# Optimization experiments

Hardware: AMD Instinct MI355X
Metric: run time of the kernel (lower is better)

Reference implementation:

```python
import jax, jax.numpy as jnp
import numpy as np

WINDOW_SIZE = 11
CHANNEL = 3
SIGMA = 1.5


def _make_window(w=WINDOW_SIZE, channel=CHANNEL, sigma=SIGMA):
    xs = np.arange(w) - w // 2
    g = np.exp(-(xs.astype(np.float64) ** 2) / (2.0 * sigma ** 2))
    g = g / g.sum()
    k2d = np.outer(g, g).astype(np.float32)  # [w,w]
    # depthwise kernel, OIHW with I=1, O=channel
    return jnp.asarray(np.broadcast_to(k2d, (channel, 1, w, w)).copy())


def setup_inputs() -> dict:
    key = jax.random.key(0)
    k1, k2 = jax.random.split(key)
    x = jax.random.uniform(k1, (32, 3, 512, 512), dtype=jnp.float32)
    y = jax.random.uniform(k2, (32, 3, 512, 512), dtype=jnp.float32)
    window = _make_window()
    return {"x": x, "y": y, "window": window}


def _dwconv(x, window):
    pad = WINDOW_SIZE // 2
    return jax.lax.conv_general_dilated(
        x, window,
        window_strides=(1, 1),
        padding=[(pad, pad), (pad, pad)],
        dimension_numbers=("NCHW", "OIHW", "NCHW"),
        feature_group_count=CHANNEL,
    )


def reference(x, y, window):
    C1 = 0.01 ** 2
    C2 = 0.03 ** 2
    mu_x = _dwconv(x, window)
    mu_y = _dwconv(y, window)
    mu_x2 = mu_x * mu_x
    mu_y2 = mu_y * mu_y
    mu_xy = mu_x * mu_y
    sigma_x2 = _dwconv(x * x, window) - mu_x2
    sigma_y2 = _dwconv(y * y, window) - mu_y2
    sigma_xy = _dwconv(x * y, window) - mu_xy
    ssim_map = ((2.0 * mu_xy + C1) * (2.0 * sigma_xy + C2)) / (
        (mu_x2 + mu_y2 + C1) * (sigma_x2 + sigma_y2 + C2)
    )
    return jnp.mean(ssim_map)
```

## Files before the change

### kernel.cpp

```cpp
#include <hip/hip_runtime.h>


#define NBLK  768
#define NSTEP 74

__device__ __forceinline__ float2 f2z() { return make_float2(0.f, 0.f); }

#define DECL_ACC(S) float2 AX##S=f2z(), AY##S=f2z(), AXX##S=f2z(), AYY##S=f2z(), AXY##S=f2z();

#define HTAP(J, EA, EB) { const float gj = g[J]; \
  { const float xv = x##EA, yv = y##EA; const float t1 = gj*xv, t2 = gj*yv; \
    sxA += t1; syA += t2; sxxA = fmaf(t1,xv,sxxA); syyA = fmaf(t2,yv,syyA); sxyA = fmaf(t1,yv,sxyA); } \
  { const float xv = x##EB, yv = y##EB; const float t1 = gj*xv, t2 = gj*yv; \
    sxB += t1; syB += t2; sxxB = fmaf(t1,xv,sxxB); syyB = fmaf(t2,yv,syyB); sxyB = fmaf(t1,yv,sxyB); } }

#define VACC(S, RR) { const float wj = g[(10 - (S) + (RR)) % 11]; \
  AX##S.x  = fmaf(wj, sxA , AX##S.x ); AX##S.y  = fmaf(wj, sxB , AX##S.y ); \
  AY##S.x  = fmaf(wj, syA , AY##S.x ); AY##S.y  = fmaf(wj, syB , AY##S.y ); \
  AXX##S.x = fmaf(wj, sxxA, AXX##S.x); AXX##S.y = fmaf(wj, sxxB, AXX##S.y); \
  AYY##S.x = fmaf(wj, syyA, AYY##S.x); AYY##S.y = fmaf(wj, syyB, AYY##S.y); \
  AXY##S.x = fmaf(wj, sxyA, AXY##S.x); AXY##S.y = fmaf(wj, sxyB, AXY##S.y); }

#define EMIT(S) { \
  { const float mux = AX##S.x, muy = AY##S.x; \
    const float mux2 = mux*mux, muy2 = muy*muy, muxy = mux*muy; \
    const float vvx = AXX##S.x - mux2, vvy = AYY##S.x - muy2, vxy = AXY##S.x - muxy; \
    const float num = fmaf(2.f, muxy, C1) * fmaf(2.f, vxy, C2); \
    const float den = (mux2 + muy2 + C1) * (vvx + vvy + C2); \
    ts.x += num * __builtin_amdgcn_rcpf(den); } \
  { const float mux = AX##S.y, muy = AY##S.y; \
    const float mux2 = mux*mux, muy2 = muy*muy, muxy = mux*muy; \
    const float vvx = AXX##S.y - mux2, vvy = AYY##S.y - muy2, vxy = AXY##S.y - muxy; \
    const float num = fmaf(2.f, muxy, C1) * fmaf(2.f, vxy, C2); \
    const float den = (mux2 + muy2 + C1) * (vvx + vvy + C2); \
    ts.y += num * __builtin_amdgcn_rcpf(den); } }

#define RESET(S) { AX##S=f2z(); AY##S=f2z(); AXX##S=f2z(); AYY##S=f2z(); AXY##S=f2z(); }

#define STEP(RR) { \
  const int i = ibase + (RR); \
  if (i < NSTEP) { \
    const int rn = r0 - 4 + i; \
    float2 mx=f2z(), my=f2z(), hx=f2z(), hy=f2z(); \
    if (i <= NSTEP-2 && (unsigned)rn < 512u) { \
      const float* xp = xplane + rn * 512; \
      const float* yp = yplane + rn * 512; \
      mx = *(const float2*)(xp + mcol); my = *(const float2*)(yp + mcol); \
      if (hOK) { hx = *(const float2*)(xp + hcol); hy = *(const float2*)(yp + hcol); } \
    } \
    const float2 xa0 = sxw[lane  ], xa1 = sxw[lane+1], xa2 = sxw[lane+2], xa3 = sxw[lane+3]; \
    const float2 xa4 = sxw[lane+4], xa5 = sxw[lane+5], xa6 = sxw[lane+6]; \
    const float2 ya0 = syw[lane  ], ya1 = syw[lane+1], ya2 = syw[lane+2], ya3 = syw[lane+3]; \
    const float2 ya4 = syw[lane+4], ya5 = syw[lane+5], ya6 = syw[lane+6]; \
    float sxA=0.f, syA=0.f, sxxA=0.f, syyA=0.f, sxyA=0.f; \
    float sxB=0.f, syB=0.f, sxxB=0.f, syyB=0.f, sxyB=0.f; \
    HTAP(0,a0.y,a1.x) HTAP(1,a1.x,a1.y) HTAP(2,a1.y,a2.x) HTAP(3,a2.x,a2.y) \
    HTAP(4,a2.y,a3.x) HTAP(5,a3.x,a3.y) HTAP(6,a3.y,a4.x) HTAP(7,a4.x,a4.y) \
    HTAP(8,a4.y,a5.x) HTAP(9,a5.x,a5.y) HTAP(10,a5.y,a6.x) \
    VACC(0,RR) VACC(1,RR) VACC(2,RR) VACC(3,RR) VACC(4,RR) VACC(5,RR) \
    VACC(6,RR) VACC(7,RR) VACC(8,RR) VACC(9,RR) VACC(10,RR) \
    if (i >= 10) { EMIT(RR) } \
    RESET(RR) \
    sxw[lane+3] = mx; syw[lane+3] = my; \
    if (isHalo) { sxw[hslot] = hx; syw[hslot] = hy; } \
  } }

__global__ __launch_bounds__(256, 2) void ssim_fused(
    const float* __restrict__ x, const float* __restrict__ y,
    const float* __restrict__ window,
    unsigned* __restrict__ counter, float* __restrict__ partials,
    float* __restrict__ out)
{
    const int tid  = threadIdx.x;
    const int lane = tid & 63;
    const int wv   = tid >> 6;
    const int W    = blockIdx.x * 4 + wv;
    const int img  = W >> 5;
    const int cb   = (W >> 3) & 3;
    const int rb   = W & 7;
    const int r0   = rb << 6;
    const int c0   = cb << 7;

    const float* xplane = x + (size_t)img * 262144;
    const float* yplane = y + (size_t)img * 262144;

    float g[11];
    #pragma unroll
    for (int ii = 0; ii < 11; ++ii) {
        float s = 0.f;
        #pragma unroll
        for (int jj = 0; jj < 11; ++jj) s += window[ii * 11 + jj];
        g[ii] = s;
    }

    __shared__ float2 lsx[4][70];
    __shared__ float2 lsy[4][70];
    float2* sxw = lsx[wv];
    float2* syw = lsy[wv];

    const bool isHalo = lane < 6;
    const int  hslot  = (lane < 3) ? lane : (64 + lane);
    const int  hcol   = (lane < 3) ? (c0 - 6 + 2 * lane)
                                   : (c0 + 128 + 2 * (lane - 3));
    const bool hOK    = isHalo && (hcol >= 0) && (hcol < 511);
    const int  mcol   = c0 + 2 * lane;

    DECL_ACC(0) DECL_ACC(1) DECL_ACC(2) DECL_ACC(3) DECL_ACC(4) DECL_ACC(5)
    DECL_ACC(6) DECL_ACC(7) DECL_ACC(8) DECL_ACC(9) DECL_ACC(10)

    {
        const int rn = r0 - 5;
        float2 mx = f2z(), my = f2z(), hx = f2z(), hy = f2z();
        if (rn >= 0) {
            const float* xp = xplane + rn * 512;
            const float* yp = yplane + rn * 512;
            mx = *(const float2*)(xp + mcol);
            my = *(const float2*)(yp + mcol);
            if (hOK) { hx = *(const float2*)(xp + hcol); hy = *(const float2*)(yp + hcol); }
        }
        sxw[lane + 3] = mx; syw[lane + 3] = my;
        if (isHalo) { sxw[hslot] = hx; syw[hslot] = hy; }
    }

    float2 ts = f2z();
    const float C1 = 1e-4f, C2 = 9e-4f;

    #pragma unroll 1
    for (int chunk = 0; chunk < 7; ++chunk) {
        const int ibase = chunk * 11;
        STEP(0) STEP(1) STEP(2) STEP(3) STEP(4) STEP(5)
        STEP(6) STEP(7) STEP(8) STEP(9) STEP(10)
    }

    float t = ts.x + ts.y;
    #pragma unroll
    for (int off = 32; off > 0; off >>= 1) t += __shfl_down(t, off, 64);
    __shared__ float wsum[4];
    __shared__ int   sflag;
    if (lane == 0) wsum[wv] = t;
    __syncthreads();
    if (tid == 0) {
        partials[blockIdx.x] = (wsum[0] + wsum[1]) + (wsum[2] + wsum[3]);
        __threadfence();
        const unsigned old = atomicAdd(counter, 1u);
        sflag = (old == NBLK - 1) ? 1 : 0;
    }
    __syncthreads();
    if (sflag) {
        __threadfence();
        double s = 0.0;
        for (int idx = tid; idx < NBLK; idx += 256) s += (double)partials[idx];
        #pragma unroll
        for (int off = 32; off > 0; off >>= 1) s += __shfl_down(s, off, 64);
        __shared__ double dsum[4];
        if (lane == 0) dsum[wv] = s;
        __syncthreads();
        if (tid == 0)
            out[0] = (float)(((dsum[0] + dsum[1]) + (dsum[2] + dsum[3])) / 25165824.0);
    }
}

extern "C" void kernel_launch(void* const* d_in, const int* in_sizes, int n_in,
                              void* d_out, int out_size, void* d_ws, size_t ws_size,
                              hipStream_t stream)
{
    const float* x = (const float*)d_in[0];
    const float* y = (const float*)d_in[1];
    const float* w = (const float*)d_in[2];
    unsigned* counter = (unsigned*)d_ws;
    float* partials   = (float*)((char*)d_ws + 256);

    hipMemsetAsync(d_ws, 0, 4, stream);
    ssim_fused<<<NBLK, 256, 0, stream>>>(x, y, w, counter, partials, (float*)d_out);
}
```

Baseline: 305.9 us.

## Use one-wave blocks with scalar Gaussian weights and wave-level final reduction

Changes the launch from 768 blocks of four waves to 3072 single-wave blocks, with each block owning one 64x128 tile. The Gaussian weights become named scalars broadcast via readfirstlane, and the vertical-tap index is resolved per step at preprocessing time, so weights can sit in SGPRs instead of a runtime-indexed array. Block-level shared-memory reductions and __syncthreads are replaced by a shuffle broadcast of the atomic counter result. Dropping the (256,2) launch bound frees the register budget, which may change occupancy. Four times as many partials must be summed in the final pass.

```diff
diff --git a/kernel.cpp b/kernel.cpp
--- a/kernel.cpp
+++ b/kernel.cpp
@@ -1,25 +1,38 @@
 #include <hip/hip_runtime.h>
 
 
-#define NBLK  768
+#define NBLK  3072
 #define NSTEP 74
 
 __device__ __forceinline__ float2 f2z() { return make_float2(0.f, 0.f); }
 
 #define DECL_ACC(S) float2 AX##S=f2z(), AY##S=f2z(), AXX##S=f2z(), AYY##S=f2z(), AXY##S=f2z();
 
-#define HTAP(J, EA, EB) { const float gj = g[J]; \
+#define HTAP(J, EA, EB) { const float gj = g##J; \
   { const float xv = x##EA, yv = y##EA; const float t1 = gj*xv, t2 = gj*yv; \
     sxA += t1; syA += t2; sxxA = fmaf(t1,xv,sxxA); syyA = fmaf(t2,yv,syyA); sxyA = fmaf(t1,yv,sxyA); } \
   { const float xv = x##EB, yv = y##EB; const float t1 = gj*xv, t2 = gj*yv; \
     sxB += t1; syB += t2; sxxB = fmaf(t1,xv,sxxB); syyB = fmaf(t2,yv,syyB); sxyB = fmaf(t1,yv,sxyB); } }
 
-#define VACC(S, RR) { const float wj = g[(10 - (S) + (RR)) % 11]; \
+#define VACC1(S, GW) { const float wj = GW; \
   AX##S.x  = fmaf(wj, sxA , AX##S.x ); AX##S.y  = fmaf(wj, sxB , AX##S.y ); \
   AY##S.x  = fmaf(wj, syA , AY##S.x ); AY##S.y  = fmaf(wj, syB , AY##S.y ); \
   AXX##S.x = fmaf(wj, sxxA, AXX##S.x); AXX##S.y = fmaf(wj, sxxB, AXX##S.y); \
   AYY##S.x = fmaf(wj, syyA, AYY##S.x); AYY##S.y = fmaf(wj, syyB, AYY##S.y); \
   AXY##S.x = fmaf(wj, sxyA, AXY##S.x); AXY##S.y = fmaf(wj, sxyB, AXY##S.y); }
+
+#define VACC_IDX(S, K) VACC_IDX_##K(S)
+#define VACC_IDX_0(S)  VACC1(S, g0)
+#define VACC_IDX_1(S)  VACC1(S, g1)
+#define VACC_IDX_2(S)  VACC1(S, g2)
+#define VACC_IDX_3(S)  VACC1(S, g3)
+#define VACC_IDX_4(S)  VACC1(S, g4)
+#define VACC_IDX_5(S)  VACC1(S, g5)
+#define VACC_IDX_6(S)  VACC1(S, g6)
+#define VACC_IDX_7(S)  VACC1(S, g7)
+#define VACC_IDX_8(S)  VACC1(S, g8)
+#define VACC_IDX_9(S)  VACC1(S, g9)
+#define VACC_IDX_10(S) VACC1(S, g10)
 
 #define EMIT(S) { \
   { const float mux = AX##S.x, muy = AY##S.x; \
@@ -27,13 +40,13 @@
     const float vvx = AXX##S.x - mux2, vvy = AYY##S.x - muy2, vxy = AXY##S.x - muxy; \
     const float num = fmaf(2.f, muxy, C1) * fmaf(2.f, vxy, C2); \
     const float den = (mux2 + muy2 + C1) * (vvx + vvy + C2); \
-    ts.x += num * __builtin_amdgcn_rcpf(den); } \
+    tsx += num * __builtin_amdgcn_rcpf(den); } \
   { const float mux = AX##S.y, muy = AY##S.y; \
     const float mux2 = mux*mux, muy2 = muy*muy, muxy = mux*muy; \
     const float vvx = AXX##S.y - mux2, vvy = AYY##S.y - muy2, vxy = AXY##S.y - muxy; \
     const float num = fmaf(2.f, muxy, C1) * fmaf(2.f, vxy, C2); \
     const float den = (mux2 + muy2 + C1) * (vvx + vvy + C2); \
-    ts.y += num * __builtin_amdgcn_rcpf(den); } }
+    tsy += num * __builtin_amdgcn_rcpf(den); } }
 
 #define RESET(S) { AX##S=f2z(); AY##S=f2z(); AXX##S=f2z(); AYY##S=f2z(); AXY##S=f2z(); }
 
@@ -57,24 +70,33 @@
     HTAP(0,a0.y,a1.x) HTAP(1,a1.x,a1.y) HTAP(2,a1.y,a2.x) HTAP(3,a2.x,a2.y) \
     HTAP(4,a2.y,a3.x) HTAP(5,a3.x,a3.y) HTAP(6,a3.y,a4.x) HTAP(7,a4.x,a4.y) \
     HTAP(8,a4.y,a5.x) HTAP(9,a5.x,a5.y) HTAP(10,a5.y,a6.x) \
-    VACC(0,RR) VACC(1,RR) VACC(2,RR) VACC(3,RR) VACC(4,RR) VACC(5,RR) \
-    VACC(6,RR) VACC(7,RR) VACC(8,RR) VACC(9,RR) VACC(10,RR) \
+    VACC_STEP_##RR \
     if (i >= 10) { EMIT(RR) } \
     RESET(RR) \
     sxw[lane+3] = mx; syw[lane+3] = my; \
     if (isHalo) { sxw[hslot] = hx; syw[hslot] = hy; } \
   } }
 
-__global__ __launch_bounds__(256, 2) void ssim_fused(
+#define VACC_STEP_0  VACC_IDX(0,10) VACC_IDX(1,9)  VACC_IDX(2,8)  VACC_IDX(3,7)  VACC_IDX(4,6)  VACC_IDX(5,5)  VACC_IDX(6,4)  VACC_IDX(7,3)  VACC_IDX(8,2)  VACC_IDX(9,1)  VACC_IDX(10,0)
+#define VACC_STEP_1  VACC_IDX(0,0)  VACC_IDX(1,10) VACC_IDX(2,9)  VACC_IDX(3,8)  VACC_IDX(4,7)  VACC_IDX(5,6)  VACC_IDX(6,5)  VACC_IDX(7,4)  VACC_IDX(8,3)  VACC_IDX(9,2)  VACC_IDX(10,1)
+#define VACC_STEP_2  VACC_IDX(0,1)  VACC_IDX(1,0)  VACC_IDX(2,10) VACC_IDX(3,9)  VACC_IDX(4,8)  VACC_IDX(5,7)  VACC_IDX(6,6)  VACC_IDX(7,5)  VACC_IDX(8,4)  VACC_IDX(9,3)  VACC_IDX(10,2)
+#define VACC_STEP_3  VACC_IDX(0,2)  VACC_IDX(1,1)  VACC_IDX(2,0)  VACC_IDX(3,10) VACC_IDX(4,9)  VACC_IDX(5,8)  VACC_IDX(6,7)  VACC_IDX(7,6)  VACC_IDX(8,5)  VACC_IDX(9,4)  VACC_IDX(10,3)
+#define VACC_STEP_4  VACC_IDX(0,3)  VACC_IDX(1,2)  VACC_IDX(2,1)  VACC_IDX(3,0)  VACC_IDX(4,10) VACC_IDX(5,9)  VACC_IDX(6,8)  VACC_IDX(7,7)  VACC_IDX(8,6)  VACC_IDX(9,5)  VACC_IDX(10,4)
+#define VACC_STEP_5  VACC_IDX(0,4)  VACC_IDX(1,3)  VACC_IDX(2,2)  VACC_IDX(3,1)  VACC_IDX(4,0)  VACC_IDX(5,10) VACC_IDX(6,9)  VACC_IDX(7,8)  VACC_IDX(8,7)  VACC_IDX(9,6)  VACC_IDX(10,5)
+#define VACC_STEP_6  VACC_IDX(0,5)  VACC_IDX(1,4)  VACC_IDX(2,3)  VACC_IDX(3,2)  VACC_IDX(4,1)  VACC_IDX(5,0)  VACC_IDX(6,10) VACC_IDX(7,9)  VACC_IDX(8,8)  VACC_IDX(9,7)  VACC_IDX(10,6)
+#define VACC_STEP_7  VACC_IDX(0,6)  VACC_IDX(1,5)  VACC_IDX(2,4)  VACC_IDX(3,3)  VACC_IDX(4,2)  VACC_IDX(5,1)  VACC_IDX(6,0)  VACC_IDX(7,10) VACC_IDX(8,9)  VACC_IDX(9,8)  VACC_IDX(10,7)
+#define VACC_STEP_8  VACC_IDX(0,7)  VACC_IDX(1,6)  VACC_IDX(2,5)  VACC_IDX(3,4)  VACC_IDX(4,3)  VACC_IDX(5,2)  VACC_IDX(6,1)  VACC_IDX(7,0)  VACC_IDX(8,10) VACC_IDX(9,9)  VACC_IDX(10,8)
+#define VACC_STEP_9  VACC_IDX(0,8)  VACC_IDX(1,7)  VACC_IDX(2,6)  VACC_IDX(3,5)  VACC_IDX(4,4)  VACC_IDX(5,3)  VACC_IDX(6,2)  VACC_IDX(7,1)  VACC_IDX(8,0)  VACC_IDX(9,10) VACC_IDX(10,9)
+#define VACC_STEP_10 VACC_IDX(0,9)  VACC_IDX(1,8)  VACC_IDX(2,7)  VACC_IDX(3,6)  VACC_IDX(4,5)  VACC_IDX(5,4)  VACC_IDX(6,3)  VACC_IDX(7,2)  VACC_IDX(8,1)  VACC_IDX(9,0)  VACC_IDX(10,10)
+
+__global__ __launch_bounds__(64) void ssim_fused(
     const float* __restrict__ x, const float* __restrict__ y,
     const float* __restrict__ window,
     unsigned* __restrict__ counter, float* __restrict__ partials,
     float* __restrict__ out)
 {
-    const int tid  = threadIdx.x;
-    const int lane = tid & 63;
-    const int wv   = tid >> 6;
-    const int W    = blockIdx.x * 4 + wv;
+    const int lane = threadIdx.x;
+    const int W    = blockIdx.x;
     const int img  = W >> 5;
     const int cb   = (W >> 3) & 3;
     const int rb   = W & 7;
@@ -84,19 +106,19 @@
     const float* xplane = x + (size_t)img * 262144;
     const float* yplane = y + (size_t)img * 262144;
 
-    float g[11];
+    float gtmp[11];
     #pragma unroll
     for (int ii = 0; ii < 11; ++ii) {
         float s = 0.f;
         #pragma unroll
         for (int jj = 0; jj < 11; ++jj) s += window[ii * 11 + jj];
-        g[ii] = s;
+        gtmp[ii] = s;
     }
+    #define SG(N) const float g##N = __uint_as_float(__builtin_amdgcn_readfirstlane(__float_as_uint(gtmp[N])));
+    SG(0) SG(1) SG(2) SG(3) SG(4) SG(5) SG(6) SG(7) SG(8) SG(9) SG(10)
 
-    __shared__ float2 lsx[4][70];
-    __shared__ float2 lsy[4][70];
-    float2* sxw = lsx[wv];
-    float2* syw = lsy[wv];
+    __shared__ float2 sxw[70];
+    __shared__ float2 syw[70];
 
     const bool isHalo = lane < 6;
     const int  hslot  = (lane < 3) ? lane : (64 + lane);
@@ -122,7 +144,7 @@
         if (isHalo) { sxw[hslot] = hx; syw[hslot] = hy; }
     }
 
-    float2 ts = f2z();
+    float tsx = 0.f, tsy = 0.f;
     const float C1 = 1e-4f, C2 = 9e-4f;
 
     #pragma unroll 1
@@ -132,31 +154,23 @@
         STEP(6) STEP(7) STEP(8) STEP(9) STEP(10)
     }
 
-    float t = ts.x + ts.y;
+    float t = tsx + tsy;
     #pragma unroll
     for (int off = 32; off > 0; off >>= 1) t += __shfl_down(t, off, 64);
-    __shared__ float wsum[4];
-    __shared__ int   sflag;
-    if (lane == 0) wsum[wv] = t;
-    __syncthreads();
-    if (tid == 0) {
-        partials[blockIdx.x] = (wsum[0] + wsum[1]) + (wsum[2] + wsum[3]);
+    unsigned old = 0u;
+    if (lane == 0) {
+        partials[W] = t;
         __threadfence();
-        const unsigned old = atomicAdd(counter, 1u);
-        sflag = (old == NBLK - 1) ? 1 : 0;
+        old = atomicAdd(counter, 1u);
     }
-    __syncthreads();
-    if (sflag) {
+    old = __shfl(old, 0, 64);
+    if (old == NBLK - 1) {
         __threadfence();
         double s = 0.0;
-        for (int idx = tid; idx < NBLK; idx += 256) s += (double)partials[idx];
+        for (int idx = lane; idx < NBLK; idx += 64) s += (double)partials[idx];
         #pragma unroll
         for (int off = 32; off > 0; off >>= 1) s += __shfl_down(s, off, 64);
-        __shared__ double dsum[4];
-        if (lane == 0) dsum[wv] = s;
-        __syncthreads();
-        if (tid == 0)
-            out[0] = (float)(((dsum[0] + dsum[1]) + (dsum[2] + dsum[3])) / 25165824.0);
+        if (lane == 0) out[0] = (float)(s / 25165824.0);
     }
 }
 
@@ -171,5 +185,5 @@
     float* partials   = (float*)((char*)d_ws + 256);
 
     hipMemsetAsync(d_ws, 0, 4, stream);
-    ssim_fused<<<NBLK, 256, 0, stream>>>(x, y, w, counter, partials, (float*)d_out);
+    ssim_fused<<<NBLK, 64, 0, stream>>>(x, y, w, counter, partials, (float*)d_out);
 }
```

Result: slower. 370.0 us (+20.9%).

## Use shift-register vertical accumulators and triple-buffered row prefetch in SSIM kernel

Applied to the files above, without the earlier changes.

Replaces the 11-slot rotating vertical accumulator scheme with a shift-register chain that keeps ten partial sums per statistic, so each row needs only a single FMA per tap instead of updating all 11 accumulators. Global row loads are issued two steps ahead through three rotating prefetch registers. Loads become branch-free by clamping indices and masking with multipliers. Also merges the x/y LDS rows into one float4 array and makes the Gaussian weights wave-uniform via readfirstlane. The deeper prefetch adds register pressure and some redundant clamped loads at image borders, and the loop now runs 75 steps with the final ones doing extra work.

```diff
diff --git a/kernel.cpp b/kernel.cpp
--- a/kernel.cpp
+++ b/kernel.cpp
@@ -1,69 +1,71 @@
 #include <hip/hip_runtime.h>
 
 
-#define NBLK  768
-#define NSTEP 74
+#define NBLK 768
 
 __device__ __forceinline__ float2 f2z() { return make_float2(0.f, 0.f); }
-
-#define DECL_ACC(S) float2 AX##S=f2z(), AY##S=f2z(), AXX##S=f2z(), AYY##S=f2z(), AXY##S=f2z();
-
-#define HTAP(J, EA, EB) { const float gj = g[J]; \
-  { const float xv = x##EA, yv = y##EA; const float t1 = gj*xv, t2 = gj*yv; \
-    sxA += t1; syA += t2; sxxA = fmaf(t1,xv,sxxA); syyA = fmaf(t2,yv,syyA); sxyA = fmaf(t1,yv,sxyA); } \
-  { const float xv = x##EB, yv = y##EB; const float t1 = gj*xv, t2 = gj*yv; \
-    sxB += t1; syB += t2; sxxB = fmaf(t1,xv,sxxB); syyB = fmaf(t2,yv,syyB); sxyB = fmaf(t1,yv,sxyB); } }
-
-#define VACC(S, RR) { const float wj = g[(10 - (S) + (RR)) % 11]; \
-  AX##S.x  = fmaf(wj, sxA , AX##S.x ); AX##S.y  = fmaf(wj, sxB , AX##S.y ); \
-  AY##S.x  = fmaf(wj, syA , AY##S.x ); AY##S.y  = fmaf(wj, syB , AY##S.y ); \
-  AXX##S.x = fmaf(wj, sxxA, AXX##S.x); AXX##S.y = fmaf(wj, sxxB, AXX##S.y); \
-  AYY##S.x = fmaf(wj, syyA, AYY##S.x); AYY##S.y = fmaf(wj, syyB, AYY##S.y); \
-  AXY##S.x = fmaf(wj, sxyA, AXY##S.x); AXY##S.y = fmaf(wj, sxyB, AXY##S.y); }
-
-#define EMIT(S) { \
-  { const float mux = AX##S.x, muy = AY##S.x; \
-    const float mux2 = mux*mux, muy2 = muy*muy, muxy = mux*muy; \
-    const float vvx = AXX##S.x - mux2, vvy = AYY##S.x - muy2, vxy = AXY##S.x - muxy; \
-    const float num = fmaf(2.f, muxy, C1) * fmaf(2.f, vxy, C2); \
-    const float den = (mux2 + muy2 + C1) * (vvx + vvy + C2); \
-    ts.x += num * __builtin_amdgcn_rcpf(den); } \
-  { const float mux = AX##S.y, muy = AY##S.y; \
-    const float mux2 = mux*mux, muy2 = muy*muy, muxy = mux*muy; \
-    const float vvx = AXX##S.y - mux2, vvy = AYY##S.y - muy2, vxy = AXY##S.y - muxy; \
-    const float num = fmaf(2.f, muxy, C1) * fmaf(2.f, vxy, C2); \
-    const float den = (mux2 + muy2 + C1) * (vvx + vvy + C2); \
-    ts.y += num * __builtin_amdgcn_rcpf(den); } }
-
-#define RESET(S) { AX##S=f2z(); AY##S=f2z(); AXX##S=f2z(); AYY##S=f2z(); AXY##S=f2z(); }
-
-#define STEP(RR) { \
-  const int i = ibase + (RR); \
-  if (i < NSTEP) { \
-    const int rn = r0 - 4 + i; \
-    float2 mx=f2z(), my=f2z(), hx=f2z(), hy=f2z(); \
-    if (i <= NSTEP-2 && (unsigned)rn < 512u) { \
-      const float* xp = xplane + rn * 512; \
-      const float* yp = yplane + rn * 512; \
-      mx = *(const float2*)(xp + mcol); my = *(const float2*)(yp + mcol); \
-      if (hOK) { hx = *(const float2*)(xp + hcol); hy = *(const float2*)(yp + hcol); } \
-    } \
-    const float2 xa0 = sxw[lane  ], xa1 = sxw[lane+1], xa2 = sxw[lane+2], xa3 = sxw[lane+3]; \
-    const float2 xa4 = sxw[lane+4], xa5 = sxw[lane+5], xa6 = sxw[lane+6]; \
-    const float2 ya0 = syw[lane  ], ya1 = syw[lane+1], ya2 = syw[lane+2], ya3 = syw[lane+3]; \
-    const float2 ya4 = syw[lane+4], ya5 = syw[lane+5], ya6 = syw[lane+6]; \
-    float sxA=0.f, syA=0.f, sxxA=0.f, syyA=0.f, sxyA=0.f; \
-    float sxB=0.f, syB=0.f, sxxB=0.f, syyB=0.f, sxyB=0.f; \
-    HTAP(0,a0.y,a1.x) HTAP(1,a1.x,a1.y) HTAP(2,a1.y,a2.x) HTAP(3,a2.x,a2.y) \
-    HTAP(4,a2.y,a3.x) HTAP(5,a3.x,a3.y) HTAP(6,a3.y,a4.x) HTAP(7,a4.x,a4.y) \
-    HTAP(8,a4.y,a5.x) HTAP(9,a5.x,a5.y) HTAP(10,a5.y,a6.x) \
-    VACC(0,RR) VACC(1,RR) VACC(2,RR) VACC(3,RR) VACC(4,RR) VACC(5,RR) \
-    VACC(6,RR) VACC(7,RR) VACC(8,RR) VACC(9,RR) VACC(10,RR) \
-    if (i >= 10) { EMIT(RR) } \
-    RESET(RR) \
-    sxw[lane+3] = mx; syw[lane+3] = my; \
-    if (isHalo) { sxw[hslot] = hx; syw[hslot] = hy; } \
-  } }
+__device__ __forceinline__ float2 fma2(float s, float2 a, float2 c) {
+    return make_float2(fmaf(s, a.x, c.x), fmaf(s, a.y, c.y));
+}
+__device__ __forceinline__ float2 mul2(float s, float2 a) {
+    return make_float2(s * a.x, s * a.y);
+}
+
+#define DECL_CH(C) float2 C##0=f2z(),C##1=f2z(),C##2=f2z(),C##3=f2z(),C##4=f2z(), \
+                          C##5=f2z(),C##6=f2z(),C##7=f2z(),C##8=f2z(),C##9=f2z();
+#define SHIFT(C, H) \
+  C##9 = fma2(g9, H, C##8); C##8 = fma2(g8, H, C##7); C##7 = fma2(g7, H, C##6); \
+  C##6 = fma2(g6, H, C##5); C##5 = fma2(g5, H, C##4); C##4 = fma2(g4, H, C##3); \
+  C##3 = fma2(g3, H, C##2); C##2 = fma2(g2, H, C##1); C##1 = fma2(g1, H, C##0); \
+  C##0 = mul2(g0, H);
+
+#define HTAP(J, UA, UB) { const float gj = g##J; \
+  { const float xv = XV##UA, yv = YV##UA; const float t1 = gj*xv, t2 = gj*yv; \
+    HX.x += t1; HY.x += t2; HXX.x = fmaf(t1,xv,HXX.x); HYY.x = fmaf(t2,yv,HYY.x); HXY.x = fmaf(t1,yv,HXY.x); } \
+  { const float xv = XV##UB, yv = YV##UB; const float t1 = gj*xv, t2 = gj*yv; \
+    HX.y += t1; HY.y += t2; HXX.y = fmaf(t1,xv,HXX.y); HYY.y = fmaf(t2,yv,HYY.y); HXY.y = fmaf(t1,yv,HXY.y); } }
+
+#define SSIM_COL(MU_X, MU_Y, SXX, SYY, SXY, TS) { \
+  const float mux = MU_X, muy = MU_Y; \
+  const float mux2 = mux*mux, muy2 = muy*muy, muxy = mux*muy; \
+  const float vvx = SXX - mux2, vvy = SYY - muy2, vxy = SXY - muxy; \
+  const float num = fmaf(2.f, muxy, C1) * fmaf(2.f, vxy, C2); \
+  const float den = (mux2 + muy2 + C1) * (vvx + vvy + C2); \
+  TS += num * __builtin_amdgcn_rcpf(den); }
+
+#define STEP(I, P, Q) { \
+  const int i_ = (I); \
+  const int rl = r0 - 2 + i_; \
+  VM##P = ((unsigned)rl < 512u) ? 1.f : 0.f; \
+  { const int rlc = (rl < 0) ? 0 : ((rl > 511) ? 511 : rl); \
+    const float* xp = xplane + (rlc << 9); \
+    const float* yp = yplane + (rlc << 9); \
+    PF##P##mx = *(const float2*)(xp + mcol); PF##P##my = *(const float2*)(yp + mcol); \
+    PF##P##hx = *(const float2*)(xp + hcolC); PF##P##hy = *(const float2*)(yp + hcolC); } \
+  const float4 q0 = lsw[lane  ], q1 = lsw[lane+1], q2 = lsw[lane+2], q3 = lsw[lane+3]; \
+  const float4 q4 = lsw[lane+4], q5 = lsw[lane+5], q6 = lsw[lane+6]; \
+  const float XV1 = q0.y, XV2 = q1.x, XV3 = q1.y, XV4 = q2.x, XV5 = q2.y, XV6 = q3.x; \
+  const float XV7 = q3.y, XV8 = q4.x, XV9 = q4.y, XV10 = q5.x, XV11 = q5.y, XV12 = q6.x; \
+  const float YV1 = q0.w, YV2 = q1.z, YV3 = q1.w, YV4 = q2.z, YV5 = q2.w, YV6 = q3.z; \
+  const float YV7 = q3.w, YV8 = q4.z, YV9 = q4.w, YV10 = q5.z, YV11 = q5.w, YV12 = q6.z; \
+  float2 HX = f2z(), HY = f2z(), HXX = f2z(), HYY = f2z(), HXY = f2z(); \
+  HTAP(0,1,2)  HTAP(1,2,3)  HTAP(2,3,4)  HTAP(3,4,5)  HTAP(4,5,6)  HTAP(5,6,7) \
+  HTAP(6,7,8)  HTAP(7,8,9)  HTAP(8,9,10) HTAP(9,10,11) HTAP(10,11,12) \
+  if (i_ >= 10 && i_ < 74) { \
+    const float2 EX  = fma2(g10, HX , CX9 ); \
+    const float2 EY  = fma2(g10, HY , CY9 ); \
+    const float2 EXX = fma2(g10, HXX, CXX9); \
+    const float2 EYY = fma2(g10, HYY, CYY9); \
+    const float2 EXY = fma2(g10, HXY, CXY9); \
+    SSIM_COL(EX.x, EY.x, EXX.x, EYY.x, EXY.x, tsx) \
+    SSIM_COL(EX.y, EY.y, EXX.y, EYY.y, EXY.y, tsy) \
+  } \
+  SHIFT(CX, HX) SHIFT(CY, HY) SHIFT(CXX, HXX) SHIFT(CYY, HYY) SHIFT(CXY, HXY) \
+  { const float fq = VM##Q; const float fh = fq * hmask; \
+    const float2 wmx = mul2(fq, PF##Q##mx), wmy = mul2(fq, PF##Q##my); \
+    const float2 whx = mul2(fh, PF##Q##hx), why = mul2(fh, PF##Q##hy); \
+    lsw[lane + 3] = make_float4(wmx.x, wmx.y, wmy.x, wmy.y); \
+    if (lane < 6) lsw[hslot] = make_float4(whx.x, whx.y, why.x, why.y); } }
 
 __global__ __launch_bounds__(256, 2) void ssim_fused(
     const float* __restrict__ x, const float* __restrict__ y,
@@ -84,55 +86,78 @@
     const float* xplane = x + (size_t)img * 262144;
     const float* yplane = y + (size_t)img * 262144;
 
-    float g[11];
+    const int  hslot = (lane < 3) ? lane : (64 + lane);
+    const int  hcol  = (lane < 3) ? (c0 - 6 + 2 * lane)
+                                  : (c0 + 128 + 2 * (lane - 3));
+    const float hmask = (lane < 6 && hcol >= 0 && hcol < 511) ? 1.f : 0.f;
+    const int  hcolC = (hcol < 0) ? 0 : ((hcol > 510) ? 510 : hcol);
+    const int  mcol  = c0 + 2 * lane;
+
+    float gtmp[11];
     #pragma unroll
     for (int ii = 0; ii < 11; ++ii) {
         float s = 0.f;
         #pragma unroll
         for (int jj = 0; jj < 11; ++jj) s += window[ii * 11 + jj];
-        g[ii] = s;
-    }
-
-    __shared__ float2 lsx[4][70];
-    __shared__ float2 lsy[4][70];
-    float2* sxw = lsx[wv];
-    float2* syw = lsy[wv];
-
-    const bool isHalo = lane < 6;
-    const int  hslot  = (lane < 3) ? lane : (64 + lane);
-    const int  hcol   = (lane < 3) ? (c0 - 6 + 2 * lane)
-                                   : (c0 + 128 + 2 * (lane - 3));
-    const bool hOK    = isHalo && (hcol >= 0) && (hcol < 511);
-    const int  mcol   = c0 + 2 * lane;
-
-    DECL_ACC(0) DECL_ACC(1) DECL_ACC(2) DECL_ACC(3) DECL_ACC(4) DECL_ACC(5)
-    DECL_ACC(6) DECL_ACC(7) DECL_ACC(8) DECL_ACC(9) DECL_ACC(10)
+        gtmp[ii] = s;
+    }
+    #define SG(N) const float g##N = __uint_as_float(__builtin_amdgcn_readfirstlane(__float_as_uint(gtmp[N])));
+    SG(0) SG(1) SG(2) SG(3) SG(4) SG(5) SG(6) SG(7) SG(8) SG(9) SG(10)
+
+    __shared__ float4 ls4[4][72];
+    float4* lsw = ls4[wv];
+
+    DECL_CH(CX) DECL_CH(CY) DECL_CH(CXX) DECL_CH(CYY) DECL_CH(CXY)
+
+    float2 PF0mx, PF0my, PF0hx, PF0hy; float VM0 = 0.f;
+    float2 PF1mx, PF1my, PF1hx, PF1hy; float VM1;
+    float2 PF2mx, PF2my, PF2hx, PF2hy; float VM2;
 
     {
-        const int rn = r0 - 5;
-        float2 mx = f2z(), my = f2z(), hx = f2z(), hy = f2z();
-        if (rn >= 0) {
-            const float* xp = xplane + rn * 512;
-            const float* yp = yplane + rn * 512;
-            mx = *(const float2*)(xp + mcol);
-            my = *(const float2*)(yp + mcol);
-            if (hOK) { hx = *(const float2*)(xp + hcol); hy = *(const float2*)(yp + hcol); }
-        }
-        sxw[lane + 3] = mx; syw[lane + 3] = my;
-        if (isHalo) { sxw[hslot] = hx; syw[hslot] = hy; }
-    }
-
-    float2 ts = f2z();
+        const int rl = r0 - 5;
+        const float fq = ((unsigned)rl < 512u) ? 1.f : 0.f;
+        const int rlc = (rl < 0) ? 0 : rl;
+        const float* xp = xplane + (rlc << 9);
+        const float* yp = yplane + (rlc << 9);
+        const float2 mx = *(const float2*)(xp + mcol), my = *(const float2*)(yp + mcol);
+        const float2 hx = *(const float2*)(xp + hcolC), hy = *(const float2*)(yp + hcolC);
+        const float fh = fq * hmask;
+        const float2 wmx = mul2(fq, mx), wmy = mul2(fq, my);
+        const float2 whx = mul2(fh, hx), why = mul2(fh, hy);
+        lsw[lane + 3] = make_float4(wmx.x, wmx.y, wmy.x, wmy.y);
+        if (lane < 6) lsw[hslot] = make_float4(whx.x, whx.y, why.x, why.y);
+    }
+    {
+        const int rl = r0 - 4;
+        VM1 = ((unsigned)rl < 512u) ? 1.f : 0.f;
+        const int rlc = (rl < 0) ? 0 : rl;
+        const float* xp = xplane + (rlc << 9);
+        const float* yp = yplane + (rlc << 9);
+        PF1mx = *(const float2*)(xp + mcol); PF1my = *(const float2*)(yp + mcol);
+        PF1hx = *(const float2*)(xp + hcolC); PF1hy = *(const float2*)(yp + hcolC);
+    }
+    {
+        const int rl = r0 - 3;
+        VM2 = ((unsigned)rl < 512u) ? 1.f : 0.f;
+        const int rlc = (rl < 0) ? 0 : rl;
+        const float* xp = xplane + (rlc << 9);
+        const float* yp = yplane + (rlc << 9);
+        PF2mx = *(const float2*)(xp + mcol); PF2my = *(const float2*)(yp + mcol);
+        PF2hx = *(const float2*)(xp + hcolC); PF2hy = *(const float2*)(yp + hcolC);
+    }
+
+    float tsx = 0.f, tsy = 0.f;
     const float C1 = 1e-4f, C2 = 9e-4f;
 
     #pragma unroll 1
-    for (int chunk = 0; chunk < 7; ++chunk) {
-        const int ibase = chunk * 11;
-        STEP(0) STEP(1) STEP(2) STEP(3) STEP(4) STEP(5)
-        STEP(6) STEP(7) STEP(8) STEP(9) STEP(10)
-    }
-
-    float t = ts.x + ts.y;
+    for (int it = 0; it < 25; ++it) {
+        const int i0 = it * 3;
+        STEP(i0 + 0, 0, 1)
+        STEP(i0 + 1, 1, 2)
+        STEP(i0 + 2, 2, 0)
+    }
+
+    float t = tsx + tsy;
     #pragma unroll
     for (int off = 32; off > 0; off >>= 1) t += __shfl_down(t, off, 64);
     __shared__ float wsum[4];
```

New measurement: 282.4 us. -7.7%, faster.
